# Performance work log

Measured on AMD Instinct MI355X. Metric: run time of the kernel, lower is better.

## Reference

```python
import jax, jax.numpy as jnp
import numpy as np

N_NODES = 50000
N_EDGES = 800000
DIM = 128
HEADS = 8
DK = DIM // HEADS  # 16
SQRT_DK = float(np.sqrt(DK))


def setup_inputs() -> dict:
    key = jax.random.key(0)
    ks = jax.random.split(key, 12)
    inp = {
        "h": jax.random.normal(ks[0], (N_NODES, DIM), jnp.float32),
        "src": jax.random.randint(ks[1], (N_EDGES,), 0, N_NODES, jnp.int32),
        "dst": jax.random.randint(ks[2], (N_EDGES,), 0, N_NODES, jnp.int32),
        "Wk": jax.random.normal(ks[3], (DIM, DIM), jnp.float32) / np.sqrt(DIM),
        "bk": jnp.zeros((DIM,), jnp.float32),
        "Wq": jax.random.normal(ks[4], (DIM, DIM), jnp.float32) / np.sqrt(DIM),
        "bq": jnp.zeros((DIM,), jnp.float32),
        "Wv": jax.random.normal(ks[5], (DIM, DIM), jnp.float32) / np.sqrt(DIM),
        "bv": jnp.zeros((DIM,), jnp.float32),
        "Wa": jax.random.normal(ks[6], (DIM, DIM), jnp.float32) / np.sqrt(DIM),
        "ba": jnp.zeros((DIM,), jnp.float32),
        "rel_att": jax.random.normal(ks[7], (HEADS, DK, DK), jnp.float32) / np.sqrt(DK),
        "rel_msg": jax.random.normal(ks[8], (HEADS, DK, DK), jnp.float32) / np.sqrt(DK),
        "rel_pri": jnp.ones((HEADS,), jnp.float32),
        "skip": jnp.ones((1,), jnp.float32),
    }
    return inp


def reference(h, src, dst, Wk, bk, Wq, bq, Wv, bv, Wa, ba, rel_att, rel_msg, rel_pri, skip):
    N = h.shape[0]
    # node-level projections -> [N, H, d_k]
    k = (h @ Wk + bk).reshape(N, HEADS, DK)
    q = (h @ Wq + bq).reshape(N, HEADS, DK)
    v = (h @ Wv + bv).reshape(N, HEADS, DK)
    # relation-specific transforms
    k = jnp.einsum('nhi,hij->nhj', k, rel_att)
    v = jnp.einsum('nhi,hij->nhj', v, rel_msg)
    # per-edge score: dot(q[dst], k[src]) over d_k -> [E, H]
    score = jnp.einsum('ehd,ehd->eh', q[dst], k[src]) * rel_pri / SQRT_DK
    # segment softmax over destination nodes (edge_softmax, norm_by='dst')
    smax = jax.ops.segment_max(score, dst, num_segments=N)  # [N, H]
    e = jnp.exp(score - smax[dst])
    ssum = jax.ops.segment_sum(e, dst, num_segments=N)  # [N, H]
    attn = e / ssum[dst]  # [E, H]
    # weighted scatter-sum of messages: sum_e v[src_e] * attn_e -> [N, H, d_k]
    m = v[src] * attn[:, :, None]
    t = jax.ops.segment_sum(m, dst, num_segments=N).reshape(N, DIM)
    # target-specific aggregation (dropout in eval mode = identity, use_norm=False)
    trans_out = t @ Wa + ba
    alpha = jax.nn.sigmoid(skip)  # [1], broadcasts
    new_h = trans_out * alpha + h * (1.0 - alpha)
    return new_h
```

## Files before the change

kernel.cpp:

```cpp
#include <hip/hip_runtime.h>
#include <stdint.h>

#define NN 50000
#define NE 800000

typedef __bf16 v8bf __attribute__((ext_vector_type(8)));
typedef float  v4f  __attribute__((ext_vector_type(4)));

#define EXP2F(x) __builtin_amdgcn_exp2f(x)

__device__ __forceinline__ float bf2f(unsigned short u) {
    return __uint_as_float(((unsigned)u) << 16);
}
__device__ __forceinline__ unsigned short f2bf(float f) {
    unsigned u = __float_as_uint(f);
    u += 0x7FFFu + ((u >> 16) & 1u);
    return (unsigned short)(u >> 16);
}
__device__ __forceinline__ float ldf(const void* p, size_t i, int isb) {
    return isb ? bf2f(((const unsigned short*)p)[i]) : ((const float*)p)[i];
}

__global__ __launch_bounds__(128) void k_prep(
    const void* __restrict__ Wq, const void* __restrict__ bq,
    const void* __restrict__ Wk, const void* __restrict__ bk,
    const void* __restrict__ Wv, const void* __restrict__ bv,
    const void* __restrict__ Wa, const void* __restrict__ ba,
    const void* __restrict__ rel_att, const void* __restrict__ rel_msg,
    const void* __restrict__ rel_pri, const int* __restrict__ dst,
    unsigned* __restrict__ CNT,
    int* __restrict__ FLAG, unsigned short* __restrict__ WTb,
    float* __restrict__ BC)
{
    int b = blockIdx.x;
    int j = threadIdx.x;
    if (b >= 512) {
        int e = (b - 512) * 128 + j;
        atomicAdd(&CNT[dst[e]], 1u);
        return;
    }
    const unsigned rp0 = ((const unsigned*)rel_pri)[0];
    const int isb = ((rp0 & 0xFFFFu) != 0u) ? 1 : 0;
    int m = b >> 7;
    int i = b & 127;
    if (b == 0 && j == 0) FLAG[0] = isb;
    if (m == 0) {
        WTb[((size_t)(0 * 128 + j)) * 128 + i] = f2bf(ldf(Wq, i * 128 + j, isb));
        if (i == 0) BC[j] = ldf(bq, j, isb);
    } else if (m == 3) {
        WTb[((size_t)(3 * 128 + j)) * 128 + i] = f2bf(ldf(Wa, i * 128 + j, isb));
        if (i == 0) BC[3 * 128 + j] = ldf(ba, j, isb);
    } else {
        const void* W    = (m == 1) ? Wk : Wv;
        const void* bias = (m == 1) ? bk : bv;
        const void* R    = (m == 1) ? rel_att : rel_msg;
        int hh = j >> 4, jj = j & 15;
        float scale = (m == 1) ? ldf(rel_pri, hh, isb) * 0.25f : 1.0f;
        float acc = 0.f, bacc = 0.f;
        #pragma unroll
        for (int l = 0; l < 16; ++l) {
            float r = ldf(R, hh * 256 + l * 16 + jj, isb);
            acc  += ldf(W, i * 128 + hh * 16 + l, isb) * r;
            bacc += ldf(bias, hh * 16 + l, isb) * r;
        }
        WTb[((size_t)(m * 128 + j)) * 128 + i] = f2bf(acc * scale);
        if (i == 0) BC[m * 128 + j] = bacc * scale;
    }
}

__global__ __launch_bounds__(256) void k_qkv(
    const void* __restrict__ h, const unsigned short* __restrict__ WTb,
    const float* __restrict__ BC, const int* __restrict__ FLAG,
    unsigned short* __restrict__ Qb, unsigned short* __restrict__ KVb)
{
    __shared__ __align__(16) unsigned short Ah[64][136];
    __shared__ __align__(16) unsigned short Bh[128][136];
    const int isb = FLAG[0];
    const int tid = threadIdx.x;
    const int rowBase = blockIdx.x * 64;

    if (isb) {
        #pragma unroll
        for (int i = 0; i < 4; ++i) {
            int lin = tid + i * 256;
            int row = lin >> 4, kc = (lin & 15) * 8;
            int gr = rowBase + row;
            uint4 u = make_uint4(0, 0, 0, 0);
            if (gr < NN) u = *(const uint4*)((const unsigned short*)h + (size_t)gr * 128 + kc);
            *(uint4*)&Ah[row][kc] = u;
        }
    } else {
        #pragma unroll
        for (int i = 0; i < 8; ++i) {
            int lin = tid + i * 256;
            int row = lin >> 5, c4 = (lin & 31) * 4;
            int gr = rowBase + row;
            ushort4 o = make_ushort4(0, 0, 0, 0);
            if (gr < NN) {
                float4 f = *(const float4*)((const float*)h + (size_t)gr * 128 + c4);
                o.x = f2bf(f.x); o.y = f2bf(f.y); o.z = f2bf(f.z); o.w = f2bf(f.w);
            }
            *(ushort4*)&Ah[row][c4] = o;
        }
    }

    const int w = tid >> 6, l = tid & 63;
    const int lr = l & 15, q = l >> 4;
    v4f accK[8];

    for (int m = 0; m < 3; ++m) {
        if (m) __syncthreads();
        #pragma unroll
        for (int i = 0; i < 8; ++i) {
            int lin = tid + i * 256;
            int col = lin >> 4, kc = (lin & 15) * 8;
            uint4 u = *(const uint4*)(WTb + ((size_t)(m * 128 + col)) * 128 + kc);
            *(uint4*)&Bh[col][kc] = u;
        }
        __syncthreads();

        v4f acc[8];
        #pragma unroll
        for (int nt = 0; nt < 8; ++nt) {
            float bj = BC[m * 128 + nt * 16 + lr];
            acc[nt] = (v4f){bj, bj, bj, bj};
        }
        #pragma unroll
        for (int kk = 0; kk < 4; ++kk) {
            v8bf a = *(const v8bf*)&Ah[w * 16 + lr][kk * 32 + q * 8];
            #pragma unroll
            for (int nt = 0; nt < 8; ++nt) {
                v8bf b = *(const v8bf*)&Bh[nt * 16 + lr][kk * 32 + q * 8];
                acc[nt] = __builtin_amdgcn_mfma_f32_16x16x32_bf16(a, b, acc[nt], 0, 0, 0);
            }
        }
        if (m == 0) {
            #pragma unroll
            for (int nt = 0; nt < 8; ++nt)
                #pragma unroll
                for (int r = 0; r < 4; ++r) {
                    int row = rowBase + w * 16 + q * 4 + r;
                    if (row < NN)
                        Qb[(size_t)row * 128 + nt * 16 + lr] = f2bf(acc[nt][r]);
                }
        } else if (m == 1) {
            #pragma unroll
            for (int nt = 0; nt < 8; ++nt) accK[nt] = acc[nt];
        } else {
            #pragma unroll
            for (int nt = 0; nt < 8; ++nt)
                #pragma unroll
                for (int r = 0; r < 4; ++r) {
                    int row = rowBase + w * 16 + q * 4 + r;
                    if (row < NN) {
                        ushort2 kv;
                        kv.x = f2bf(accK[nt][r]);
                        kv.y = f2bf(acc[nt][r]);
                        *(ushort2*)&KVb[(size_t)row * 256 + (nt * 16 + lr) * 2] = kv;
                    }
                }
        }
    }
}

#define SCB 512
#define NSB 98
__global__ __launch_bounds__(SCB) void k_scan(
    const unsigned* __restrict__ CNT, unsigned* __restrict__ RPS,
    unsigned* __restrict__ BSUM, unsigned* __restrict__ BOFF,
    unsigned* __restrict__ DONE, unsigned* __restrict__ CUR)
{
    __shared__ unsigned sh[SCB];
    __shared__ int lastFlag;
    int tid = threadIdx.x;
    int g = blockIdx.x * SCB + tid;
    if (g < 50048) CUR[g] = 0u;
    unsigned v = (g < NN) ? CNT[g] : 0u;
    sh[tid] = v;
    __syncthreads();
    #pragma unroll
    for (int off = 1; off < SCB; off <<= 1) {
        unsigned t = 0;
        if (tid >= off) t = sh[tid - off];
        __syncthreads();
        if (tid >= off) sh[tid] += t;
        __syncthreads();
    }
    if (g < NN) RPS[g] = sh[tid] - v;
    if (tid == SCB - 1) atomicExch(&BSUM[blockIdx.x], sh[tid]);
    __syncthreads();
    if (tid == 0) {
        __threadfence();
        lastFlag = (atomicAdd(DONE, 1u) == NSB - 1);
    }
    __syncthreads();
    if (!lastFlag) return;

    unsigned bv = (tid < NSB) ? atomicAdd(&BSUM[tid], 0u) : 0u;
    sh[tid] = bv;
    __syncthreads();
    #pragma unroll
    for (int off = 1; off < SCB; off <<= 1) {
        unsigned t = 0;
        if (tid >= off) t = sh[tid - off];
        __syncthreads();
        if (tid >= off) sh[tid] += t;
        __syncthreads();
    }
    if (tid < NSB) BOFF[tid] = sh[tid] - bv;
}

__global__ __launch_bounds__(256) void k_fill(
    const int* __restrict__ src, const int* __restrict__ dst,
    const unsigned* __restrict__ RPS, const unsigned* __restrict__ BOFF,
    unsigned* __restrict__ CUR, int* __restrict__ ESRC)
{
    int e = blockIdx.x * 256 + threadIdx.x;
    int d = dst[e];
    int pos = (int)atomicAdd(&CUR[d], 1u);
    ESRC[(int)(RPS[d] + BOFF[d >> 9]) + pos] = src[e];
}

__global__ __launch_bounds__(256) void k_attn(
    const unsigned* __restrict__ RPS, const unsigned* __restrict__ BOFF,
    const int* __restrict__ ESRC,
    const unsigned short* __restrict__ Qb, const unsigned short* __restrict__ KVb,
    unsigned short* __restrict__ Tb)
{
    int d = (blockIdx.x * 256 + threadIdx.x) >> 6;
    int lane = threadIdx.x & 63;
    int beg = (int)(RPS[d] + BOFF[d >> 9]);
    int end = (d == NN - 1) ? NE : (int)(RPS[d + 1] + BOFF[(d + 1) >> 9]);
    const float LOG2E = 1.4426950408889634f;

    ushort2 qq = *(const ushort2*)(Qb + (size_t)d * 128 + lane * 2);
    float q0 = bf2f(qq.x) * LOG2E, q1 = bf2f(qq.y) * LOG2E;

    float s = 0.f, o0 = 0.f, o1 = 0.f;
    for (int j = beg; j < end; j += 8) {
        ushort4 kv[8];
        #pragma unroll
        for (int t = 0; t < 8; ++t) {
            int idx = j + t;
            int sid = ESRC[(idx < end) ? idx : (end - 1)];
            kv[t] = *(const ushort4*)(KVb + (size_t)sid * 256 + lane * 4);
        }
        #pragma unroll
        for (int t = 0; t < 8; ++t) {
            float p = q0 * bf2f(kv[t].x) + q1 * bf2f(kv[t].z);
            p += __shfl_xor(p, 1);
            p += __shfl_xor(p, 2);
            p += __shfl_xor(p, 4);
            float w = (j + t < end) ? EXP2F(p) : 0.f;
            s  += w;
            o0 += w * bf2f(kv[t].y);
            o1 += w * bf2f(kv[t].w);
        }
    }
    float r = (s > 0.f) ? (1.0f / s) : 0.f;
    ushort2 o;
    o.x = f2bf(o0 * r); o.y = f2bf(o1 * r);
    *(ushort2*)(Tb + (size_t)d * 128 + lane * 2) = o;
}

__global__ __launch_bounds__(256) void k_final_m(
    const unsigned short* __restrict__ Tb, const unsigned short* __restrict__ WTb,
    const float* __restrict__ BC, const void* __restrict__ h,
    const void* __restrict__ skip, const int* __restrict__ FLAG,
    void* __restrict__ out)
{
    __shared__ __align__(16) unsigned short Ah[64][136];
    __shared__ __align__(16) unsigned short Bh[128][136];
    const int isb = FLAG[0];
    const int tid = threadIdx.x;
    const int rowBase = blockIdx.x * 64;

    #pragma unroll
    for (int i = 0; i < 4; ++i) {
        int lin = tid + i * 256;
        int row = lin >> 4, kc = (lin & 15) * 8;
        int gr = rowBase + row;
        uint4 u = make_uint4(0, 0, 0, 0);
        if (gr < NN) u = *(const uint4*)(Tb + (size_t)gr * 128 + kc);
        *(uint4*)&Ah[row][kc] = u;
    }
    #pragma unroll
    for (int i = 0; i < 8; ++i) {
        int lin = tid + i * 256;
        int col = lin >> 4, kc = (lin & 15) * 8;
        uint4 u = *(const uint4*)(WTb + ((size_t)(3 * 128 + col)) * 128 + kc);
        *(uint4*)&Bh[col][kc] = u;
    }
    __syncthreads();

    const int w = tid >> 6, l = tid & 63;
    const int lr = l & 15, q = l >> 4;
    v4f acc[8];
    #pragma unroll
    for (int nt = 0; nt < 8; ++nt) {
        float bj = BC[3 * 128 + nt * 16 + lr];
        acc[nt] = (v4f){bj, bj, bj, bj};
    }
    #pragma unroll
    for (int kk = 0; kk < 4; ++kk) {
        v8bf a = *(const v8bf*)&Ah[w * 16 + lr][kk * 32 + q * 8];
        #pragma unroll
        for (int nt = 0; nt < 8; ++nt) {
            v8bf b = *(const v8bf*)&Bh[nt * 16 + lr][kk * 32 + q * 8];
            acc[nt] = __builtin_amdgcn_mfma_f32_16x16x32_bf16(a, b, acc[nt], 0, 0, 0);
        }
    }
    float skipv = ldf(skip, 0, isb);
    float alpha = 1.0f / (1.0f + __expf(-skipv));
    float beta = 1.0f - alpha;
    #pragma unroll
    for (int nt = 0; nt < 8; ++nt) {
        #pragma unroll
        for (int r = 0; r < 4; ++r) {
            int row = rowBase + w * 16 + q * 4 + r;
            if (row < NN) {
                size_t off = (size_t)row * 128 + nt * 16 + lr;
                float hv = ldf(h, off, isb);
                float o = alpha * acc[nt][r] + beta * hv;
                if (isb) ((unsigned short*)out)[off] = f2bf(o);
                else     ((float*)out)[off] = o;
            }
        }
    }
}

extern "C" void kernel_launch(void* const* d_in, const int* in_sizes, int n_in,
                              void* d_out, int out_size, void* d_ws, size_t ws_size,
                              hipStream_t stream)
{
    const void* h  = d_in[0];
    const int* src = (const int*)d_in[1];
    const int* dst = (const int*)d_in[2];
    const void* Wk = d_in[3];
    const void* bk = d_in[4];
    const void* Wq = d_in[5];
    const void* bq = d_in[6];
    const void* Wv = d_in[7];
    const void* bv = d_in[8];
    const void* Wa = d_in[9];
    const void* ba = d_in[10];
    const void* rel_att = d_in[11];
    const void* rel_msg = d_in[12];
    const void* rel_pri = d_in[13];
    const void* skip    = d_in[14];

    float* F = (float*)d_ws;
    int* FLAG      = (int*)F;
    float* BC      = F + 16;
    unsigned short* WTb = (unsigned short*)(BC + 512);
    unsigned* CNT  = (unsigned*)((float*)(BC + 512) + 32768);
    unsigned* DONE = CNT + 50048;
    unsigned* CUR  = DONE + 16;
    unsigned* RPS  = CUR + 50048;
    unsigned* BSUM = RPS + 50048;
    unsigned* BOFF = BSUM + 128;
    unsigned short* Tb = (unsigned short*)(BOFF + 128);
    int* ESRC      = (int*)(Tb + (size_t)NN * 128);
    unsigned short* Qb  = (unsigned short*)(ESRC + NE);
    unsigned short* KVb = Qb + (size_t)NN * 128;

    (void)hipMemsetAsync(CNT, 0, (50048 + 16) * sizeof(unsigned), stream);

    k_prep<<<512 + 6250, 128, 0, stream>>>(Wq, bq, Wk, bk, Wv, bv, Wa, ba,
                                           rel_att, rel_msg, rel_pri, dst, CNT,
                                           FLAG, WTb, BC);
    k_qkv<<<782, 256, 0, stream>>>(h, WTb, BC, FLAG, Qb, KVb);
    k_scan<<<NSB, SCB, 0, stream>>>(CNT, RPS, BSUM, BOFF, DONE, CUR);
    k_fill<<<NE / 256, 256, 0, stream>>>(src, dst, RPS, BOFF, CUR, ESRC);
    k_attn<<<(NN * 64) / 256, 256, 0, stream>>>(RPS, BOFF, ESRC, Qb, KVb, Tb);
    k_final_m<<<782, 256, 0, stream>>>(Tb, WTb, BC, h, skip, FLAG, d_out);
}
```

Measured before the change: 285.6 us.

## Pad atomic counters to 64B and process two edges per wave in attention

Degree counters and fill cursors are now spaced 16 words apart, so each node's atomic lands in its own 64-byte slot. This is meant to cut atomic contention and cache-line sharing during counting and CSR fill. The cost is a much larger memset and more cache footprint when the scan reads the strided counts. The attention kernel now splits each wave into two 32-lane halves that handle different edges with 16-byte K/V loads. The halves are combined with a cross-half shuffle at the end, which halves the loop trip count and the shuffle reductions per edge.

```diff
diff --git a/kernel.cpp b/kernel.cpp
--- a/kernel.cpp
+++ b/kernel.cpp
@@ -6,6 +6,7 @@
 
 typedef __bf16 v8bf __attribute__((ext_vector_type(8)));
 typedef float  v4f  __attribute__((ext_vector_type(4)));
+typedef unsigned short v8us __attribute__((ext_vector_type(8)));
 
 #define EXP2F(x) __builtin_amdgcn_exp2f(x)
 
@@ -28,7 +29,7 @@
     const void* __restrict__ Wa, const void* __restrict__ ba,
     const void* __restrict__ rel_att, const void* __restrict__ rel_msg,
     const void* __restrict__ rel_pri, const int* __restrict__ dst,
-    unsigned* __restrict__ CNT,
+    unsigned* __restrict__ CNTP,
     int* __restrict__ FLAG, unsigned short* __restrict__ WTb,
     float* __restrict__ BC)
 {
@@ -36,7 +37,7 @@
     int j = threadIdx.x;
     if (b >= 512) {
         int e = (b - 512) * 128 + j;
-        atomicAdd(&CNT[dst[e]], 1u);
+        atomicAdd(&CNTP[(unsigned)dst[e] << 4], 1u);
         return;
     }
     const unsigned rp0 = ((const unsigned*)rel_pri)[0];
@@ -166,16 +167,15 @@
 #define SCB 512
 #define NSB 98
 __global__ __launch_bounds__(SCB) void k_scan(
-    const unsigned* __restrict__ CNT, unsigned* __restrict__ RPS,
+    const unsigned* __restrict__ CNTP, unsigned* __restrict__ RPS,
     unsigned* __restrict__ BSUM, unsigned* __restrict__ BOFF,
-    unsigned* __restrict__ DONE, unsigned* __restrict__ CUR)
+    unsigned* __restrict__ DONE)
 {
     __shared__ unsigned sh[SCB];
     __shared__ int lastFlag;
     int tid = threadIdx.x;
     int g = blockIdx.x * SCB + tid;
-    if (g < 50048) CUR[g] = 0u;
-    unsigned v = (g < NN) ? CNT[g] : 0u;
+    unsigned v = (g < NN) ? CNTP[(size_t)g << 4] : 0u;
     sh[tid] = v;
     __syncthreads();
     #pragma unroll
@@ -213,11 +213,11 @@
 __global__ __launch_bounds__(256) void k_fill(
     const int* __restrict__ src, const int* __restrict__ dst,
     const unsigned* __restrict__ RPS, const unsigned* __restrict__ BOFF,
-    unsigned* __restrict__ CUR, int* __restrict__ ESRC)
+    unsigned* __restrict__ CURP, int* __restrict__ ESRC)
 {
     int e = blockIdx.x * 256 + threadIdx.x;
     int d = dst[e];
-    int pos = (int)atomicAdd(&CUR[d], 1u);
+    int pos = (int)atomicAdd(&CURP[(unsigned)d << 4], 1u);
     ESRC[(int)(RPS[d] + BOFF[d >> 9]) + pos] = src[e];
 }
 
@@ -229,38 +229,53 @@
 {
     int d = (blockIdx.x * 256 + threadIdx.x) >> 6;
     int lane = threadIdx.x & 63;
+    int hl = lane >> 5;
+    int sub = lane & 31;
     int beg = (int)(RPS[d] + BOFF[d >> 9]);
     int end = (d == NN - 1) ? NE : (int)(RPS[d + 1] + BOFF[(d + 1) >> 9]);
     const float LOG2E = 1.4426950408889634f;
 
-    ushort2 qq = *(const ushort2*)(Qb + (size_t)d * 128 + lane * 2);
-    float q0 = bf2f(qq.x) * LOG2E, q1 = bf2f(qq.y) * LOG2E;
-
-    float s = 0.f, o0 = 0.f, o1 = 0.f;
+    const ushort4 qu = *(const ushort4*)(Qb + (size_t)d * 128 + sub * 4);
+    float q0 = bf2f(qu.x) * LOG2E, q1 = bf2f(qu.y) * LOG2E;
+    float q2 = bf2f(qu.z) * LOG2E, q3 = bf2f(qu.w) * LOG2E;
+
+    float s = 0.f, o0 = 0.f, o1 = 0.f, o2 = 0.f, o3 = 0.f;
     for (int j = beg; j < end; j += 8) {
-        ushort4 kv[8];
-        #pragma unroll
-        for (int t = 0; t < 8; ++t) {
-            int idx = j + t;
-            int sid = ESRC[(idx < end) ? idx : (end - 1)];
-            kv[t] = *(const ushort4*)(KVb + (size_t)sid * 256 + lane * 4);
-        }
-        #pragma unroll
-        for (int t = 0; t < 8; ++t) {
-            float p = q0 * bf2f(kv[t].x) + q1 * bf2f(kv[t].z);
+        v8us kv[4];
+        int valid[4];
+        #pragma unroll
+        for (int t = 0; t < 4; ++t) {
+            int idx = j + 2 * t + hl;
+            valid[t] = idx < end;
+            int sid = ESRC[valid[t] ? idx : end - 1];
+            kv[t] = *(const v8us*)(KVb + (size_t)sid * 256 + sub * 8);
+        }
+        #pragma unroll
+        for (int t = 0; t < 4; ++t) {
+            float p = q0 * bf2f(kv[t][0]) + q1 * bf2f(kv[t][2])
+                    + q2 * bf2f(kv[t][4]) + q3 * bf2f(kv[t][6]);
             p += __shfl_xor(p, 1);
             p += __shfl_xor(p, 2);
-            p += __shfl_xor(p, 4);
-            float w = (j + t < end) ? EXP2F(p) : 0.f;
+            float w = valid[t] ? EXP2F(p) : 0.f;
             s  += w;
-            o0 += w * bf2f(kv[t].y);
-            o1 += w * bf2f(kv[t].w);
-        }
-    }
+            o0 += w * bf2f(kv[t][1]);
+            o1 += w * bf2f(kv[t][3]);
+            o2 += w * bf2f(kv[t][5]);
+            o3 += w * bf2f(kv[t][7]);
+        }
+    }
+    s  += __shfl_xor(s, 32);
+    o0 += __shfl_xor(o0, 32);
+    o1 += __shfl_xor(o1, 32);
+    o2 += __shfl_xor(o2, 32);
+    o3 += __shfl_xor(o3, 32);
     float r = (s > 0.f) ? (1.0f / s) : 0.f;
-    ushort2 o;
-    o.x = f2bf(o0 * r); o.y = f2bf(o1 * r);
-    *(ushort2*)(Tb + (size_t)d * 128 + lane * 2) = o;
+    if (hl == 0) {
+        ushort4 o;
+        o.x = f2bf(o0 * r); o.y = f2bf(o1 * r);
+        o.z = f2bf(o2 * r); o.w = f2bf(o3 * r);
+        *(ushort4*)(Tb + (size_t)d * 128 + sub * 4) = o;
+    }
 }
 
 __global__ __launch_bounds__(256) void k_final_m(
@@ -353,10 +368,10 @@
     int* FLAG      = (int*)F;
     float* BC      = F + 16;
     unsigned short* WTb = (unsigned short*)(BC + 512);
-    unsigned* CNT  = (unsigned*)((float*)(BC + 512) + 32768);
-    unsigned* DONE = CNT + 50048;
-    unsigned* CUR  = DONE + 16;
-    unsigned* RPS  = CUR + 50048;
+    unsigned* CNTP = (unsigned*)((float*)(BC + 512) + 32768);
+    unsigned* CURP = CNTP + 800000;
+    unsigned* DONE = CURP + 800000;
+    unsigned* RPS  = DONE + 16;
     unsigned* BSUM = RPS + 50048;
     unsigned* BOFF = BSUM + 128;
     unsigned short* Tb = (unsigned short*)(BOFF + 128);
@@ -364,14 +379,14 @@
     unsigned short* Qb  = (unsigned short*)(ESRC + NE);
     unsigned short* KVb = Qb + (size_t)NN * 128;
 
-    (void)hipMemsetAsync(CNT, 0, (50048 + 16) * sizeof(unsigned), stream);
+    (void)hipMemsetAsync(CNTP, 0, (800000 + 800000 + 16) * sizeof(unsigned), stream);
 
     k_prep<<<512 + 6250, 128, 0, stream>>>(Wq, bq, Wk, bk, Wv, bv, Wa, ba,
-                                           rel_att, rel_msg, rel_pri, dst, CNT,
+                                           rel_att, rel_msg, rel_pri, dst, CNTP,
                                            FLAG, WTb, BC);
     k_qkv<<<782, 256, 0, stream>>>(h, WTb, BC, FLAG, Qb, KVb);
-    k_scan<<<NSB, SCB, 0, stream>>>(CNT, RPS, BSUM, BOFF, DONE, CUR);
-    k_fill<<<NE / 256, 256, 0, stream>>>(src, dst, RPS, BOFF, CUR, ESRC);
+    k_scan<<<NSB, SCB, 0, stream>>>(CNTP, RPS, BSUM, BOFF, DONE);
+    k_fill<<<NE / 256, 256, 0, stream>>>(src, dst, RPS, BOFF, CURP, ESRC);
     k_attn<<<(NN * 64) / 256, 256, 0, stream>>>(RPS, BOFF, ESRC, Qb, KVb, Tb);
     k_final_m<<<782, 256, 0, stream>>>(Tb, WTb, BC, h, skip, FLAG, d_out);
 }
```

After: 281.2 us. No clear change (-1.5%).
